# Kernel optimization log

Measured on AMD Instinct MI355X. Metric: run time of the kernel, lower is better.

## Reference

```python
import jax, jax.numpy as jnp
import numpy as np

B, S, D, H = 4, 4096, 1024, 16
DK = D // H
EPS = 1e-6

def _feature_map(x):
    # ELU + 1 -> strictly positive features
    return jax.nn.elu(x) + 1.0

def setup_inputs() -> dict:
    key = jax.random.key(0)
    ks = jax.random.split(key, 11)
    s = 1.0 / np.sqrt(D)
    return {
        "query": jax.random.normal(ks[0], (B, S, D), jnp.float32),
        "key":   jax.random.normal(ks[1], (B, S, D), jnp.float32),
        "value": jax.random.normal(ks[2], (B, S, D), jnp.float32),
        "Wq": jax.random.uniform(ks[3], (D, D), jnp.float32, -s, s),
        "bq": jax.random.uniform(ks[4], (D,), jnp.float32, -s, s),
        "Wk": jax.random.uniform(ks[5], (D, D), jnp.float32, -s, s),
        "bk": jax.random.uniform(ks[6], (D,), jnp.float32, -s, s),
        "Wv": jax.random.uniform(ks[7], (D, D), jnp.float32, -s, s),
        "bv": jax.random.uniform(ks[8], (D,), jnp.float32, -s, s),
        "Wo": jax.random.uniform(ks[9], (D, D), jnp.float32, -s, s),
        "bo": jax.random.uniform(ks[10], (D,), jnp.float32, -s, s),
    }

def reference(query, key, value, Wq, bq, Wk, bk, Wv, bv, Wo, bo):
    def heads(x, W, b):
        # torch Linear: x @ W.T + b, then split heads -> [B, H, S, DK]
        y = x @ W.T + b
        return y.reshape(B, S, H, DK).transpose(0, 2, 1, 3)

    Q = _feature_map(heads(query, Wq, bq))
    K = _feature_map(heads(key, Wk, bk))
    V = heads(value, Wv, bv)

    # KV[b,h,m,d] = sum_n K[b,h,n,d] * V[b,h,n,m]  (d: K feat dim, m: V dim)
    KV = jnp.einsum('bhnd,bhnm->bhmd', K, V)
    # normalizer Z[b,h,n] = Q[b,h,n,:] . sum_n K
    Z = jnp.einsum('bhnd,bhd->bhn', Q, K.sum(axis=2))[..., None] + EPS
    out = jnp.einsum('bhnd,bhmd->bhnm', Q, KV) / Z  # [B,H,S,DK]
    out = out.transpose(0, 2, 1, 3).reshape(B, S, D)
    return out @ Wo.T + bo
```

## Files before the change

kernel.cpp:

```cpp
#include <hip/hip_runtime.h>
#include <math.h>

#define Bb 4
#define Ss 4096
#define Dd 1024
#define Hh 16
#define DKk 64
#define Mm (Bb * Ss)
#define NCH 16

typedef __attribute__((ext_vector_type(8))) short bf16x8;
typedef __attribute__((ext_vector_type(4))) float f32x4;

__device__ __forceinline__ unsigned short f2bf(float f) {
  unsigned u = __float_as_uint(f);
  u += 0x7FFFu + ((u >> 16) & 1u);
  return (unsigned short)(u >> 16);
}
__device__ __forceinline__ float bf2f(unsigned short s) {
  return __uint_as_float(((unsigned)s) << 16);
}
__device__ __forceinline__ unsigned cvt2(float lo, float hi) {
  unsigned r;
  asm("v_cvt_pk_bf16_f32 %0, %1, %2" : "=v"(r) : "v"(lo), "v"(hi));
  return r;
}

#define GLOAD(dst, src)                                                     \
  __builtin_amdgcn_global_load_lds(                                         \
      (const __attribute__((address_space(1))) void*)(src),                 \
      (__attribute__((address_space(3))) void*)(dst), 16, 0, 0)

__global__ __launch_bounds__(256) void cvt_f32_bf16(
    const float* __restrict__ s0, const float* __restrict__ s1,
    const float* __restrict__ s2, const float* __restrict__ s3,
    unsigned short* __restrict__ d0, unsigned short* __restrict__ d1,
    unsigned short* __restrict__ d2, unsigned short* __restrict__ d3, int n4) {
  const float* s; unsigned short* d;
  switch (blockIdx.y) {
    case 0:  s = s0; d = d0; break;
    case 1:  s = s1; d = d1; break;
    case 2:  s = s2; d = d2; break;
    default: s = s3; d = d3; break;
  }
  const int i = blockIdx.x * 256 + threadIdx.x;
  if (i < n4) {
    float4 v = ((const float4*)s)[i];
    ushort4 o;
    o.x = f2bf(v.x); o.y = f2bf(v.y); o.z = f2bf(v.z); o.w = f2bf(v.w);
    ((ushort4*)d)[i] = o;
  }
}

__global__ __launch_bounds__(256) void cvt_pk_f32_bf16(
    const float* __restrict__ s0, const float* __restrict__ s1,
    unsigned short* __restrict__ d0, unsigned short* __restrict__ d1,
    int n8) {
  const float* s = blockIdx.y ? s1 : s0;
  unsigned short* d = blockIdx.y ? d1 : d0;
  for (long i = (long)blockIdx.x * 256 + threadIdx.x; i < n8;
       i += (long)gridDim.x * 256) {
    float4 a = ((const float4*)s)[2 * i];
    float4 b = ((const float4*)s)[2 * i + 1];
    int4 w;
    w.x = cvt2(a.x, a.y); w.y = cvt2(a.z, a.w);
    w.z = cvt2(b.x, b.y); w.w = cvt2(b.z, b.w);
    ((int4*)d)[i] = w;
  }
}

#define LOADA(mh)                                                            \
  _Pragma("unroll") for (int mi = 0; mi < 4; ++mi)                           \
    _Pragma("unroll") for (int ks = 0; ks < 2; ++ks)                         \
      afr[mi][ks] = *(const bf16x8*)(bufA +                                  \
          ((mh) * 128 + wm * 64 + mi * 16 + fr) * 64 + (swz_rd ^ (ks * 32)));

#define LOADB(nh)                                                            \
  _Pragma("unroll") for (int ni = 0; ni < 2; ++ni)                           \
    _Pragma("unroll") for (int ks = 0; ks < 2; ++ks)                         \
      bvr[ni][ks] = *(const bf16x8*)(bufB +                                  \
          ((nh) * 128 + wn * 32 + ni * 16 + fr) * 64 + (swz_rd ^ (ks * 32)));

#define MFMAQ(mh, nh)                                                        \
  __builtin_amdgcn_s_setprio(1);                                             \
  _Pragma("unroll") for (int mi = 0; mi < 4; ++mi)                           \
    _Pragma("unroll") for (int ni = 0; ni < 2; ++ni)                         \
      _Pragma("unroll") for (int ks = 0; ks < 2; ++ks)                       \
        acc[(mh) * 4 + mi][(nh) * 2 + ni] =                                  \
            __builtin_amdgcn_mfma_f32_16x16x32_bf16(                         \
                afr[mi][ks], bvr[ni][ks],                                    \
                acc[(mh) * 4 + mi][(nh) * 2 + ni], 0, 0, 0);                 \
  __builtin_amdgcn_s_setprio(0);

#define SYNC_PRE_MFMA()                                                      \
  __builtin_amdgcn_s_barrier();                                              \
  asm volatile("s_waitcnt lgkmcnt(0)" ::: "memory");                         \
  __builtin_amdgcn_sched_barrier(0);

template <typename OutT>
__device__ __forceinline__ void gemm256_body(
    const unsigned short* __restrict__ A,
    const unsigned short* __restrict__ W,
    const float* __restrict__ bias,
    OutT* __restrict__ C, const int act, const int wg_in,
    unsigned short* lds) {
  const int t = threadIdx.x;
  const int wave = t >> 6, lane = t & 63;
  const int wm = wave >> 2, wn = wave & 3;
  const int fr = lane & 15, fq = lane >> 4;

  const int wg = ((wg_in & 7) << 5) | (wg_in >> 3);
  const int bm = wg >> 2, bn = wg & 3;

  f32x4 acc[8][4];
#pragma unroll
  for (int i = 0; i < 8; ++i)
#pragma unroll
    for (int j = 0; j < 4; ++j) acc[i][j] = (f32x4){0.f, 0.f, 0.f, 0.f};

  const int r = t >> 3;
  const int swz_st = ((t & 7) ^ (r & 7)) << 3;
  const unsigned short* gA[4];
  const unsigned short* gB[4];
#pragma unroll
  for (int l = 0; l < 4; ++l) {
    const int ga_row = (l & 1) * 128 + (l >> 1) * 64 + r;
    const int bb = l * 2 + (r >> 5);
    const int gb_row = (bb & 3) * 64 + (bb >> 2) * 32 + (r & 31);
    gA[l] = A + (size_t)(bm * 256 + ga_row) * Dd + swz_st;
    gB[l] = W + (size_t)(bn * 256 + gb_row) * Dd + swz_st;
  }
  const int dstoff = wave * 512;

  const int swz_rd = (fq * 8) ^ ((fr & 7) << 3);

  GLOAD(lds + 0 * 4096 + dstoff, gA[0]);
  GLOAD(lds + 1 * 4096 + dstoff, gA[1]);
  GLOAD(lds + 16384 + 0 * 4096 + dstoff, gB[0]);
  GLOAD(lds + 16384 + 1 * 4096 + dstoff, gB[1]);
  GLOAD(lds + 2 * 4096 + dstoff, gA[2]);
  GLOAD(lds + 3 * 4096 + dstoff, gA[3]);
  GLOAD(lds + 16384 + 2 * 4096 + dstoff, gB[2]);
  GLOAD(lds + 16384 + 3 * 4096 + dstoff, gB[3]);
  asm volatile("s_waitcnt vmcnt(4)" ::: "memory");
  __builtin_amdgcn_s_barrier();

  for (int tt = 0; tt < 16; ++tt) {
    unsigned short* bufA = lds + (tt & 1) * 32768;
    unsigned short* bufB = bufA + 16384;
    unsigned short* nA = lds + ((tt & 1) ^ 1) * 32768;
    unsigned short* nB = nA + 16384;
    const int kpre = (tt < 15 ? tt + 1 : 15) * 64;

    bf16x8 afr[4][2], bvr[2][2];
    LOADA(0)
    LOADB(0)
    GLOAD(nA + 0 * 4096 + dstoff, gA[0] + kpre);
    GLOAD(nA + 1 * 4096 + dstoff, gA[1] + kpre);
    GLOAD(nB + 0 * 4096 + dstoff, gB[0] + kpre);
    GLOAD(nB + 1 * 4096 + dstoff, gB[1] + kpre);
    asm volatile("s_waitcnt vmcnt(4)" ::: "memory");
    SYNC_PRE_MFMA()
    MFMAQ(0, 0)
    __builtin_amdgcn_s_barrier();
    LOADB(1)
    GLOAD(nA + 2 * 4096 + dstoff, gA[2] + kpre);
    GLOAD(nA + 3 * 4096 + dstoff, gA[3] + kpre);
    GLOAD(nB + 2 * 4096 + dstoff, gB[2] + kpre);
    GLOAD(nB + 3 * 4096 + dstoff, gB[3] + kpre);
    SYNC_PRE_MFMA()
    MFMAQ(0, 1)
    __builtin_amdgcn_s_barrier();
    LOADA(1)
    SYNC_PRE_MFMA()
    MFMAQ(1, 1)
    __builtin_amdgcn_s_barrier();
    LOADB(0)
    asm volatile("s_waitcnt vmcnt(4)" ::: "memory");
    SYNC_PRE_MFMA()
    MFMAQ(1, 0)
    __builtin_amdgcn_s_barrier();
  }

  const size_t row0 = (size_t)bm * 256 + wm * 128 + fq * 4;
  const int col0 = bn * 256 + wn * 64 + fr;
#pragma unroll
  for (int a = 0; a < 8; ++a) {
    const size_t row_a = row0 + (a >> 2) * 64 + (a & 3) * 16;
#pragma unroll
    for (int b = 0; b < 4; ++b) {
      const int col = col0 + (b >> 1) * 32 + (b & 1) * 16;
      const float bvl = bias[col];
#pragma unroll
      for (int rr2 = 0; rr2 < 4; ++rr2) {
        const size_t row = row_a + rr2;
        float vv = acc[a][b][rr2] + bvl;
        if (act) vv = (vv > 0.f) ? (vv + 1.f) : __expf(vv);
        if constexpr (sizeof(OutT) == 2)
          ((unsigned short*)C)[row * Dd + col] = f2bf(vv);
        else
          ((float*)C)[row * Dd + col] = vv;
      }
    }
  }
}

template <int ACT, typename OutT>
__global__ __launch_bounds__(512, 2) void gemm256(
    const unsigned short* __restrict__ A, const unsigned short* __restrict__ W,
    const float* __restrict__ bias, OutT* __restrict__ C) {
  __shared__ __align__(16) unsigned short lds[2 * 32768];
  gemm256_body<OutT>(A, W, bias, C, ACT,
                     blockIdx.x + gridDim.x * blockIdx.y, lds);
}

__global__ __launch_bounds__(512, 2) void gemm256_kv(
    const unsigned short* __restrict__ A0, const unsigned short* __restrict__ W0,
    const float* __restrict__ b0, unsigned short* __restrict__ C0,
    const unsigned short* __restrict__ A1, const unsigned short* __restrict__ W1,
    const float* __restrict__ b1, unsigned short* __restrict__ C1) {
  __shared__ __align__(16) unsigned short lds[2 * 32768];
  const int wg = blockIdx.x + gridDim.x * blockIdx.y;
  if (blockIdx.z == 0)
    gemm256_body<unsigned short>(A0, W0, b0, C0, 1, wg, lds);
  else
    gemm256_body<unsigned short>(A1, W1, b1, C1, 0, wg, lds);
}

__global__ __launch_bounds__(256) void kv_partial(
    const unsigned short* __restrict__ Kf, const unsigned short* __restrict__ Vf,
    float* __restrict__ part) {
  const int bx = blockIdx.x;
  const int chunk = bx % NCH;
  const int bh = bx / NCH;
  const int h = bh % Hh, b = bh / Hh;
  const int t = threadIdx.x;
  const int tm = t >> 4, td = t & 15;
  __shared__ float sK[8][64];
  __shared__ float sV[8][64];
  float acc[4][4] = {{0.f}};
  float ksr[4] = {0.f, 0.f, 0.f, 0.f};

  const int which = t >> 7;
  const int idx = t & 127;
  const int rr = idx >> 4;
  const int dpos = (idx & 15) << 2;
  const int colbase = h * DKk;
  const int rows = Ss / NCH;

  for (int n0 = 0; n0 < rows; n0 += 8) {
    const int gr = b * Ss + chunk * rows + n0 + rr;
    const unsigned short* src = which ? Vf : Kf;
    ushort4 raw = *(const ushort4*)&src[(size_t)gr * Dd + colbase + dpos];
    __syncthreads();
    float* dst = which ? &sV[rr][dpos] : &sK[rr][dpos];
    dst[0] = bf2f(raw.x); dst[1] = bf2f(raw.y);
    dst[2] = bf2f(raw.z); dst[3] = bf2f(raw.w);
    __syncthreads();
#pragma unroll
    for (int r = 0; r < 8; ++r) {
      float kv[4], vv[4];
#pragma unroll
      for (int j = 0; j < 4; ++j) kv[j] = sK[r][td * 4 + j];
#pragma unroll
      for (int i = 0; i < 4; ++i) vv[i] = sV[r][tm * 4 + i];
#pragma unroll
      for (int i = 0; i < 4; ++i)
#pragma unroll
        for (int j = 0; j < 4; ++j)
          acc[i][j] = fmaf(vv[i], kv[j], acc[i][j]);
      if (tm == 0) {
#pragma unroll
        for (int j = 0; j < 4; ++j) ksr[j] += kv[j];
      }
    }
  }

  float* p = part + (size_t)bx * 4160;
#pragma unroll
  for (int i = 0; i < 4; ++i)
#pragma unroll
    for (int j = 0; j < 4; ++j)
      p[(tm * 4 + i) * 64 + td * 4 + j] = acc[i][j];
  if (tm == 0) {
#pragma unroll
    for (int j = 0; j < 4; ++j) p[4096 + td * 4 + j] = ksr[j];
  }
}

__global__ __launch_bounds__(256) void kv_reduce(
    const float* __restrict__ part, float* __restrict__ KV,
    float* __restrict__ Ksum) {
  const int bh = blockIdx.x;
  for (int e = threadIdx.x; e < 4160; e += 256) {
    float s = 0.f;
#pragma unroll
    for (int c = 0; c < NCH; ++c)
      s += part[((size_t)bh * NCH + c) * 4160 + e];
    if (e < 4096) KV[(size_t)bh * 4096 + e] = s;
    else Ksum[bh * 64 + (e - 4096)] = s;
  }
}

__global__ __launch_bounds__(256) void attn_mfma(
    unsigned short* __restrict__ Qf, const float* __restrict__ KV,
    const float* __restrict__ Ksum) {
  const int bh = blockIdx.x;
  const int h = bh & (Hh - 1), b = bh >> 4;
  const int t = threadIdx.x;
  const int wave = t >> 6, lane = t & 63;
  const int fr = lane & 15, fq = lane >> 4;

  bf16x8 bfrag[4][2];
  const float* kvb = KV + (size_t)bh * 4096;
#pragma unroll
  for (int nj = 0; nj < 4; ++nj)
#pragma unroll
    for (int ks = 0; ks < 2; ++ks) {
      const float* src = kvb + (nj * 16 + fr) * 64 + ks * 32 + fq * 8;
      const float4 lo = *(const float4*)src;
      const float4 hi = *(const float4*)(src + 4);
      bf16x8 f;
      f[0] = (short)f2bf(lo.x); f[1] = (short)f2bf(lo.y);
      f[2] = (short)f2bf(lo.z); f[3] = (short)f2bf(lo.w);
      f[4] = (short)f2bf(hi.x); f[5] = (short)f2bf(hi.y);
      f[6] = (short)f2bf(hi.z); f[7] = (short)f2bf(hi.w);
      bfrag[nj][ks] = f;
    }
  bf16x8 zfrag[2];
#pragma unroll
  for (int ks = 0; ks < 2; ++ks) {
    bf16x8 f = (bf16x8){0, 0, 0, 0, 0, 0, 0, 0};
    if (fr == 0) {
      const float* src = Ksum + bh * 64 + ks * 32 + fq * 8;
      const float4 lo = *(const float4*)src;
      const float4 hi = *(const float4*)(src + 4);
      f[0] = (short)f2bf(lo.x); f[1] = (short)f2bf(lo.y);
      f[2] = (short)f2bf(lo.z); f[3] = (short)f2bf(lo.w);
      f[4] = (short)f2bf(hi.x); f[5] = (short)f2bf(hi.y);
      f[6] = (short)f2bf(hi.z); f[7] = (short)f2bf(hi.w);
    }
    zfrag[ks] = f;
  }

  const size_t row0 = (size_t)b * Ss + (size_t)blockIdx.y * 256 + wave * 64;
  unsigned short* qbase = Qf + row0 * Dd + h * DKk;
  bf16x8 afrag[4][2];
#pragma unroll
  for (int mi = 0; mi < 4; ++mi)
#pragma unroll
    for (int ks = 0; ks < 2; ++ks)
      afrag[mi][ks] =
          *(const bf16x8*)(qbase + (size_t)(mi * 16 + fr) * Dd + ks * 32 + fq * 8);

  f32x4 acc[4][4], zacc[4];
#pragma unroll
  for (int mi = 0; mi < 4; ++mi) {
    zacc[mi] = (f32x4){0.f, 0.f, 0.f, 0.f};
#pragma unroll
    for (int nj = 0; nj < 4; ++nj) acc[mi][nj] = (f32x4){0.f, 0.f, 0.f, 0.f};
  }
#pragma unroll
  for (int mi = 0; mi < 4; ++mi)
#pragma unroll
    for (int ks = 0; ks < 2; ++ks) {
      zacc[mi] = __builtin_amdgcn_mfma_f32_16x16x32_bf16(
          afrag[mi][ks], zfrag[ks], zacc[mi], 0, 0, 0);
#pragma unroll
      for (int nj = 0; nj < 4; ++nj)
        acc[mi][nj] = __builtin_amdgcn_mfma_f32_16x16x32_bf16(
            afrag[mi][ks], bfrag[nj][ks], acc[mi][nj], 0, 0, 0);
    }

#pragma unroll
  for (int mi = 0; mi < 4; ++mi)
#pragma unroll
    for (int r = 0; r < 4; ++r) {
      const float zv = __shfl(zacc[mi][r], lane & 48) + 1e-6f;
      const float rz = 1.0f / zv;
      const size_t ro = (size_t)(mi * 16 + fq * 4 + r) * Dd;
#pragma unroll
      for (int nj = 0; nj < 4; ++nj)
        qbase[ro + nj * 16 + fr] = f2bf(acc[mi][nj][r] * rz);
    }
}

extern "C" void kernel_launch(void* const* d_in, const int* in_sizes, int n_in,
                              void* d_out, int out_size, void* d_ws, size_t ws_size,
                              hipStream_t stream) {
  const float* q  = (const float*)d_in[0];
  const float* k  = (const float*)d_in[1];
  const float* v  = (const float*)d_in[2];
  const float* Wq = (const float*)d_in[3];
  const float* bq = (const float*)d_in[4];
  const float* Wk = (const float*)d_in[5];
  const float* bk = (const float*)d_in[6];
  const float* Wv = (const float*)d_in[7];
  const float* bv = (const float*)d_in[8];
  const float* Wo = (const float*)d_in[9];
  const float* bo = (const float*)d_in[10];
  float* out = (float*)d_out;

  unsigned short* kb  = (unsigned short*)d_ws;
  unsigned short* vb  = kb + (size_t)Mm * Dd;
  unsigned short* Kf  = vb + (size_t)Mm * Dd;
  unsigned short* Vf  = Kf + (size_t)Mm * Dd;
  unsigned short* Wqb = Vf + (size_t)Mm * Dd;
  unsigned short* Wkb = Wqb + (size_t)Dd * Dd;
  unsigned short* Wvb = Wkb + (size_t)Dd * Dd;
  unsigned short* Wob = Wvb + (size_t)Dd * Dd;
  float* KV   = (float*)(Wob + (size_t)Dd * Dd);
  float* Ksum = KV + (size_t)Bb * Hh * DKk * DKk;
  float* part = (float*)kb;

  dim3 gg(Dd / 256, Mm / 256);
  dim3 ggkv(Dd / 256, Mm / 256, 2);
  const int n8 = (Mm * Dd) / 8;

  cvt_f32_bf16<<<dim3(1024, 4), 256, 0, stream>>>(Wq, Wk, Wv, Wo, Wqb, Wkb, Wvb, Wob,
                                                  (Dd * Dd) / 4);
  cvt_pk_f32_bf16<<<dim3(2048, 2), 256, 0, stream>>>(k, v, kb, vb, n8);
  gemm256_kv<<<ggkv, 512, 0, stream>>>(kb, Wkb, bk, Kf, vb, Wvb, bv, Vf);
  kv_partial<<<Bb * Hh * NCH, 256, 0, stream>>>(Kf, Vf, part);
  kv_reduce<<<Bb * Hh, 256, 0, stream>>>(part, KV, Ksum);
  cvt_pk_f32_bf16<<<dim3(2048, 1), 256, 0, stream>>>(q, nullptr, kb, nullptr, n8);
  gemm256<1, unsigned short><<<gg, 512, 0, stream>>>(kb, Wqb, bq, Kf);
  attn_mfma<<<dim3(Bb * Hh, Ss / 256), 256, 0, stream>>>(Kf, KV, Ksum);
  gemm256<0, float><<<gg, 512, 0, stream>>>(Kf, Wob, bo, out);
}
```

Baseline: 285.3 us.

## Merge independent stages into shared launches to cut kernel count and tails

The weight conversions and the K/V input conversions now run in a single kernel. The Q input conversion runs in the same grid as the KV partial products. The KV partial reduction runs as an extra z-slice of the Q projection GEMM. Kernel launches drop from nine to six, and independent work can fill each other's idle compute units. The cost is extra early-exit blocks and some scheduling contention, and the partial buffer moves to the V-input scratch to avoid clobbering the Q input.

```diff
diff --git a/kernel.cpp b/kernel.cpp
--- a/kernel.cpp
+++ b/kernel.cpp
@@ -25,47 +25,48 @@
   asm("v_cvt_pk_bf16_f32 %0, %1, %2" : "=v"(r) : "v"(lo), "v"(hi));
   return r;
 }
+__device__ __forceinline__ void cvt8(const float* __restrict__ s,
+                                     unsigned short* __restrict__ d, long i) {
+  float4 a = ((const float4*)s)[2 * i];
+  float4 b = ((const float4*)s)[2 * i + 1];
+  int4 w;
+  w.x = cvt2(a.x, a.y); w.y = cvt2(a.z, a.w);
+  w.z = cvt2(b.x, b.y); w.w = cvt2(b.z, b.w);
+  ((int4*)d)[i] = w;
+}
 
 #define GLOAD(dst, src)                                                     \
   __builtin_amdgcn_global_load_lds(                                         \
       (const __attribute__((address_space(1))) void*)(src),                 \
       (__attribute__((address_space(3))) void*)(dst), 16, 0, 0)
 
-__global__ __launch_bounds__(256) void cvt_f32_bf16(
-    const float* __restrict__ s0, const float* __restrict__ s1,
-    const float* __restrict__ s2, const float* __restrict__ s3,
-    unsigned short* __restrict__ d0, unsigned short* __restrict__ d1,
-    unsigned short* __restrict__ d2, unsigned short* __restrict__ d3, int n4) {
-  const float* s; unsigned short* d;
-  switch (blockIdx.y) {
-    case 0:  s = s0; d = d0; break;
-    case 1:  s = s1; d = d1; break;
-    case 2:  s = s2; d = d2; break;
-    default: s = s3; d = d3; break;
-  }
-  const int i = blockIdx.x * 256 + threadIdx.x;
-  if (i < n4) {
-    float4 v = ((const float4*)s)[i];
-    ushort4 o;
-    o.x = f2bf(v.x); o.y = f2bf(v.y); o.z = f2bf(v.z); o.w = f2bf(v.w);
-    ((ushort4*)d)[i] = o;
-  }
-}
-
-__global__ __launch_bounds__(256) void cvt_pk_f32_bf16(
-    const float* __restrict__ s0, const float* __restrict__ s1,
-    unsigned short* __restrict__ d0, unsigned short* __restrict__ d1,
-    int n8) {
-  const float* s = blockIdx.y ? s1 : s0;
-  unsigned short* d = blockIdx.y ? d1 : d0;
-  for (long i = (long)blockIdx.x * 256 + threadIdx.x; i < n8;
-       i += (long)gridDim.x * 256) {
-    float4 a = ((const float4*)s)[2 * i];
-    float4 b = ((const float4*)s)[2 * i + 1];
-    int4 w;
-    w.x = cvt2(a.x, a.y); w.y = cvt2(a.z, a.w);
-    w.z = cvt2(b.x, b.y); w.w = cvt2(b.z, b.w);
-    ((int4*)d)[i] = w;
+__global__ __launch_bounds__(256) void cvt_all(
+    const float* __restrict__ k, const float* __restrict__ v,
+    const float* __restrict__ Wq, const float* __restrict__ Wk,
+    const float* __restrict__ Wv, const float* __restrict__ Wo,
+    unsigned short* __restrict__ kb, unsigned short* __restrict__ vb,
+    unsigned short* __restrict__ Wqb, unsigned short* __restrict__ Wkb,
+    unsigned short* __restrict__ Wvb, unsigned short* __restrict__ Wob) {
+  const int z = blockIdx.z;
+  if (z < 2) {
+    const float* s = z ? v : k;
+    unsigned short* d = z ? vb : kb;
+    const long n8 = ((long)Mm * Dd) / 8;
+    for (long i = (long)blockIdx.x * 256 + threadIdx.x; i < n8;
+         i += (long)gridDim.x * 256)
+      cvt8(s, d, i);
+  } else {
+    const long n8w = ((long)Dd * Dd) / 8;
+    for (long i = (long)blockIdx.x * 256 + threadIdx.x; i < 4 * n8w;
+         i += (long)gridDim.x * 256) {
+      const int which = (int)(i / n8w);
+      const long off = i - (long)which * n8w;
+      const float* s = (which == 0) ? Wq : (which == 1) ? Wk
+                       : (which == 2) ? Wv : Wo;
+      unsigned short* d = (which == 0) ? Wqb : (which == 1) ? Wkb
+                          : (which == 2) ? Wvb : Wob;
+      cvt8(s, d, off);
+    }
   }
 }
 
@@ -227,10 +228,42 @@
     gemm256_body<unsigned short>(A1, W1, b1, C1, 0, wg, lds);
 }
 
-__global__ __launch_bounds__(256) void kv_partial(
+__global__ __launch_bounds__(512, 2) void gemm256_qred(
+    const unsigned short* __restrict__ A, const unsigned short* __restrict__ W,
+    const float* __restrict__ bias, unsigned short* __restrict__ C,
+    const float* __restrict__ part, float* __restrict__ KV,
+    float* __restrict__ Ksum) {
+  __shared__ __align__(16) unsigned short lds[2 * 32768];
+  const int wg = blockIdx.x + gridDim.x * blockIdx.y;
+  if (blockIdx.z == 0) {
+    gemm256_body<unsigned short>(A, W, bias, C, 1, wg, lds);
+  } else {
+    const int bh = wg;
+    if (bh >= Bb * Hh || threadIdx.x >= 256) return;
+    for (int e = threadIdx.x; e < 4160; e += 256) {
+      float s = 0.f;
+#pragma unroll
+      for (int c = 0; c < NCH; ++c)
+        s += part[((size_t)bh * NCH + c) * 4160 + e];
+      if (e < 4096) KV[(size_t)bh * 4096 + e] = s;
+      else Ksum[bh * 64 + (e - 4096)] = s;
+    }
+  }
+}
+
+__global__ __launch_bounds__(256) void kvp_cvtq(
     const unsigned short* __restrict__ Kf, const unsigned short* __restrict__ Vf,
-    float* __restrict__ part) {
+    float* __restrict__ part,
+    const float* __restrict__ q, unsigned short* __restrict__ qb) {
+  if (blockIdx.y == 1) {
+    const long n8 = ((long)Mm * Dd) / 8;
+    for (long i = (long)blockIdx.x * 256 + threadIdx.x; i < n8;
+         i += (long)gridDim.x * 256)
+      cvt8(q, qb, i);
+    return;
+  }
   const int bx = blockIdx.x;
+  if (bx >= Bb * Hh * NCH) return;
   const int chunk = bx % NCH;
   const int bh = bx / NCH;
   const int h = bh % Hh, b = bh / Hh;
@@ -285,20 +318,6 @@
   if (tm == 0) {
 #pragma unroll
     for (int j = 0; j < 4; ++j) p[4096 + td * 4 + j] = ksr[j];
-  }
-}
-
-__global__ __launch_bounds__(256) void kv_reduce(
-    const float* __restrict__ part, float* __restrict__ KV,
-    float* __restrict__ Ksum) {
-  const int bh = blockIdx.x;
-  for (int e = threadIdx.x; e < 4160; e += 256) {
-    float s = 0.f;
-#pragma unroll
-    for (int c = 0; c < NCH; ++c)
-      s += part[((size_t)bh * NCH + c) * 4160 + e];
-    if (e < 4096) KV[(size_t)bh * 4096 + e] = s;
-    else Ksum[bh * 64 + (e - 4096)] = s;
   }
 }
 
@@ -411,20 +430,18 @@
   unsigned short* Wob = Wvb + (size_t)Dd * Dd;
   float* KV   = (float*)(Wob + (size_t)Dd * Dd);
   float* Ksum = KV + (size_t)Bb * Hh * DKk * DKk;
-  float* part = (float*)kb;
+  float* part = (float*)vb;
 
   dim3 gg(Dd / 256, Mm / 256);
-  dim3 ggkv(Dd / 256, Mm / 256, 2);
-  const int n8 = (Mm * Dd) / 8;
-
-  cvt_f32_bf16<<<dim3(1024, 4), 256, 0, stream>>>(Wq, Wk, Wv, Wo, Wqb, Wkb, Wvb, Wob,
-                                                  (Dd * Dd) / 4);
-  cvt_pk_f32_bf16<<<dim3(2048, 2), 256, 0, stream>>>(k, v, kb, vb, n8);
-  gemm256_kv<<<ggkv, 512, 0, stream>>>(kb, Wkb, bk, Kf, vb, Wvb, bv, Vf);
-  kv_partial<<<Bb * Hh * NCH, 256, 0, stream>>>(Kf, Vf, part);
-  kv_reduce<<<Bb * Hh, 256, 0, stream>>>(part, KV, Ksum);
-  cvt_pk_f32_bf16<<<dim3(2048, 1), 256, 0, stream>>>(q, nullptr, kb, nullptr, n8);
-  gemm256<1, unsigned short><<<gg, 512, 0, stream>>>(kb, Wqb, bq, Kf);
+  dim3 ggz(Dd / 256, Mm / 256, 2);
+  const int b0 = 0;
+
+  cvt_all<<<dim3(2048, 1, 3), 256, 0, stream>>>(k, v, Wq, Wk, Wv, Wo,
+                                                kb, vb, Wqb, Wkb, Wvb, Wob);
+  gemm256_kv<<<ggz, 512, 0, stream>>>(kb, Wkb, bk, Kf, vb, Wvb, bv, Vf);
+  kvp_cvtq<<<dim3(2048, 2), 256, 0, stream>>>(Kf, Vf, part, q, kb);
+  gemm256_qred<<<ggz, 512, 0, stream>>>(kb, Wqb, bq, Kf, part, KV, Ksum);
   attn_mfma<<<dim3(Bb * Hh, Ss / 256), 256, 0, stream>>>(Kf, KV, Ksum);
   gemm256<0, float><<<gg, 512, 0, stream>>>(Kf, Wob, bo, out);
-}
+  (void)b0; (void)in_sizes; (void)n_in; (void)out_size; (void)ws_size;
+}
```

Result: faster. 276.3 us (-3.2%).
